# Kernel optimization log

Measured on AMD Instinct MI355X. Metric: run time of the kernel, lower is better.

The kernel has to match this reference:

```python
import jax, jax.numpy as jnp
import numpy as np

N = 50000
E = 800000
D = 128

def setup_inputs() -> dict:
    key = jax.random.key(0)
    ks = jax.random.split(key, 10)
    s = 1.0 / np.sqrt(D)
    return {
        "hidden": jax.random.normal(ks[0], (N, D), dtype=jnp.float32),
        "edge_index": jax.random.randint(ks[1], (2, E), 0, N, dtype=jnp.int64),
        "edge_attr": jax.random.uniform(ks[2], (E, 1), dtype=jnp.float32),
        # edge_encoder: Linear(1, D)
        "We": jax.random.uniform(ks[3], (1, D), minval=-1.0, maxval=1.0, dtype=jnp.float32),
        "be": jax.random.uniform(ks[4], (D,), minval=-1.0, maxval=1.0, dtype=jnp.float32),
        # mlp: Linear(D,D) -> ReLU -> Linear(D,D); weights stored [in,out]
        "W1": jax.random.uniform(ks[5], (D, D), minval=-s, maxval=s, dtype=jnp.float32),
        "b1": jax.random.uniform(ks[6], (D,), minval=-s, maxval=s, dtype=jnp.float32),
        "W2": jax.random.uniform(ks[7], (D, D), minval=-s, maxval=s, dtype=jnp.float32),
        "b2": jax.random.uniform(ks[8], (D,), minval=-s, maxval=s, dtype=jnp.float32),
        "eps": jnp.zeros((1,), dtype=jnp.float32),
    }

def reference(hidden, edge_index, edge_attr, We, be, W1, b1, W2, b2, eps):
    # NOTE: original forward computes relu(hidden) but discards it, passing
    # raw `hidden` into the conv; replicated faithfully.
    src, dst = edge_index[0], edge_index[1]
    edge_emb = edge_attr @ We + be                      # [E, D]
    msg = jax.nn.relu(hidden[src] + edge_emb)           # gather + message
    summed = jax.ops.segment_sum(msg, dst, num_segments=N)           # [N, D]
    cnt = jax.ops.segment_sum(jnp.ones((E,), hidden.dtype), dst, num_segments=N)
    aggr = summed / jnp.maximum(cnt, 1.0)[:, None]      # scatter-mean
    h = (1.0 + eps[0]) * hidden + aggr
    h = jax.nn.relu(h @ W1 + b1)
    out = h @ W2 + b2
    return out
```

## Files before the change

kernel.cpp:

```cpp
#include <hip/hip_runtime.h>

static constexpr int N_NODES = 50000;
static constexpr int D = 128;
static constexpr int E_EDGES = 800000;
static constexpr int SLOTS = 48;
static constexpr int TILES = N_NODES / 16;

static constexpr int NB   = 256;
static constexpr int BKW  = 196;
static constexpr int CAP  = 4096;
static constexpr int EPB  = 4096;
static constexpr int ABIN = (E_EDGES + EPB - 1) / EPB;
static constexpr int ACVT = (E_EDGES + 511) / 512;
static constexpr int AWPR = 8;

using half8   = __attribute__((ext_vector_type(8))) _Float16;
using half2v  = __attribute__((ext_vector_type(2))) _Float16;
using floatx4 = __attribute__((ext_vector_type(4))) float;

__global__ __launch_bounds__(512) void bin_coarse(
    const float* __restrict__ hidden,
    const int* __restrict__ edge_index,
    const float* __restrict__ edge_attr,
    const float* __restrict__ W1, const float* __restrict__ W2,
    _Float16* __restrict__ hidden16,
    _Float16* __restrict__ W1f, _Float16* __restrict__ W2f,
    int* __restrict__ bucketFill, int2* __restrict__ coarse)
{
    const int t = threadIdx.x;
    const int b = blockIdx.x;

    if (b >= ABIN + ACVT) {
        int p = (b - ABIN - ACVT) * 512 + t;
        int lane  = p & 63;
        int ntile = (p >> 6) & 7;
        int kstep = (p >> 9) & 3;
        int mat   = p >> 11;
        const float* W = mat ? W2 : W1;
        _Float16*   Wf = mat ? W2f : W1f;
        int n     = ntile * 16 + (lane & 15);
        int kbase = kstep * 32 + (lane >> 4) * 8;
        _Float16* dst = Wf + ((size_t)((kstep * 8 + ntile) * 64 + lane)) * 8;
        #pragma unroll
        for (int j = 0; j < 8; ++j)
            dst[j] = (_Float16)W[(size_t)(kbase + j) * D + n];
        return;
    }
    if (b >= ABIN) {
        int e = (b - ABIN) * 512 + t;
        if (e < N_NODES * D / 8) {
            float4 v0 = *((const float4*)hidden + 2 * (size_t)e);
            float4 v1 = *((const float4*)hidden + 2 * (size_t)e + 1);
            half8 o;
            o[0] = (_Float16)v0.x; o[1] = (_Float16)v0.y;
            o[2] = (_Float16)v0.z; o[3] = (_Float16)v0.w;
            o[4] = (_Float16)v1.x; o[5] = (_Float16)v1.y;
            o[6] = (_Float16)v1.z; o[7] = (_Float16)v1.w;
            ((half8*)hidden16)[e] = o;
        }
        return;
    }

    __shared__ int lcnt[NB];
    __shared__ int lbase[NB];
    if (t < NB) lcnt[t] = 0;
    __syncthreads();

    const int ebase = b * EPB;
    int src[8], bk[8], dl[8], rank[8];
    float at[8];
    #pragma unroll
    for (int k = 0; k < 8; ++k) {
        int e = ebase + k * 512 + t;
        bool v = e < E_EDGES;
        int d  = v ? edge_index[E_EDGES + e] : 0;
        src[k] = v ? edge_index[e] : 0;
        at[k]  = v ? edge_attr[e] : 0.f;
        bk[k]  = (int)((unsigned)d / (unsigned)BKW);
        dl[k]  = d - bk[k] * BKW;
        rank[k] = v ? 0 : -1;
    }
    #pragma unroll
    for (int k = 0; k < 8; ++k)
        if (rank[k] >= 0)
            rank[k] = atomicAdd(&lcnt[bk[k]], 1);
    __syncthreads();

    if (t < NB) {
        int c = lcnt[t];
        lbase[t] = (c > 0) ? atomicAdd(&bucketFill[t], c) : 0;
    }
    __syncthreads();

    #pragma unroll
    for (int k = 0; k < 8; ++k) {
        if (rank[k] >= 0) {
            int idx = lbase[bk[k]] + rank[k];
            if (idx < CAP)
                coarse[(size_t)bk[k] * CAP + idx] =
                    make_int2(src[k] | (dl[k] << 16), __float_as_int(at[k]));
        }
    }
}

__global__ __launch_bounds__(512) void bin_fine(
    const int2* __restrict__ coarse,
    const int* __restrict__ bucketFill,
    int* __restrict__ counts, int2* __restrict__ csr)
{
    __shared__ int2 tile[BKW * SLOTS];
    __shared__ int  lcnt[BKW];
    const int t  = threadIdx.x;
    const int b  = blockIdx.x;
    const int n0 = b * BKW;
    const int nn = min(N_NODES - n0, BKW);

    if (t < nn) lcnt[t] = 0;
    __syncthreads();

    const int cnt = min(__builtin_amdgcn_readfirstlane(bucketFill[b]), CAP);
    const int2* seg = coarse + (size_t)b * CAP;
    for (int r = t; r < cnt; r += 512) {
        int2 rec = seg[r];
        int d   = (rec.x >> 16) & 0xff;
        int pos = atomicAdd(&lcnt[d], 1);
        if (pos < SLOTS)
            tile[d * SLOTS + pos] = make_int2(rec.x & 0xffff, rec.y);
    }
    __syncthreads();

    int4* gout = (int4*)(csr + (size_t)n0 * SLOTS);
    const int4* tin = (const int4*)tile;
    const int nq = nn * SLOTS / 2;
    for (int i = t; i < nq; i += 512)
        gout[i] = tin[i];
    if (t < nn) counts[n0 + t] = lcnt[t];
}

__global__ __launch_bounds__(256) void fused_gather_mlp(
    const _Float16* __restrict__ hidden16,
    const int2* __restrict__ csr,
    const int* __restrict__ counts,
    const float* __restrict__ We, const float* __restrict__ be,
    const float* __restrict__ eps,
    const _Float16* __restrict__ W1f, const float* __restrict__ b1,
    const _Float16* __restrict__ W2f, const float* __restrict__ b2,
    float* __restrict__ out)
{
    __shared__ _Float16 hA[16 * 136];
    __shared__ _Float16 tB[16 * 136];
    const int tid  = threadIdx.x;
    const int wave = tid >> 6;
    const int lane = tid & 63;
    const int node0 = blockIdx.x * 16;
    const int d0 = lane << 1;

    const float2 wv = *(const float2*)(We + d0);
    const float2 bv = *(const float2*)(be + d0);
    const float onePlusEps = 1.0f + eps[0];

    const int nbase = node0 + __builtin_amdgcn_readfirstlane(wave << 2);
    const int4 c4 = *(const int4*)(counts + nbase);
    int dg[4];
    dg[0] = c4.x; dg[1] = c4.y; dg[2] = c4.z; dg[3] = c4.w;

    int m_[4], mc[4];
    const int2* ep[4];
    #pragma unroll
    for (int i = 0; i < 4; ++i) {
        m_[i] = min(dg[i], SLOTS);
        mc[i] = max(m_[i] - 1, 0);
        ep[i] = csr + (size_t)(nbase + i) * SLOTS;
    }
    float a0[4] = {0.f, 0.f, 0.f, 0.f};
    float a1[4] = {0.f, 0.f, 0.f, 0.f};
    const int mmax = max(max(m_[0], m_[1]), max(m_[2], m_[3]));

    #pragma unroll 2
    for (int j = 0; j < mmax; ++j) {
        #pragma unroll
        for (int i = 0; i < 4; ++i) {
            int2 rec = ep[i][min(j, mc[i])];
            int   src = min(max(rec.x, 0), N_NODES - 1);
            float at  = __int_as_float(rec.y);
            const float g = (j < m_[i]) ? 1.0f : 0.0f;
            half2v hp = *(const half2v*)(hidden16 + (size_t)src * D + d0);
            float t0 = fmaxf((float)hp.x + __builtin_fmaf(at, wv.x, bv.x), 0.f);
            float t1 = fmaxf((float)hp.y + __builtin_fmaf(at, wv.y, bv.y), 0.f);
            a0[i] = __builtin_fmaf(g, t0, a0[i]);
            a1[i] = __builtin_fmaf(g, t1, a1[i]);
        }
    }

    #pragma unroll
    for (int i = 0; i < 4; ++i) {
        const int row = (nbase - node0) + i;
        const float rin = 1.0f / fmaxf((float)dg[i], 1.0f);
        half2v hidp = *(const half2v*)(hidden16 + (size_t)(nbase + i) * D + d0);
        half2v o;
        o.x = (_Float16)(onePlusEps * (float)hidp.x + a0[i] * rin);
        o.y = (_Float16)(onePlusEps * (float)hidp.y + a1[i] * rin);
        *(half2v*)&hA[row * 136 + d0] = o;
    }
    __syncthreads();

    const int ln16 = lane & 15;
    const int quad = lane >> 4;

    half8 a[4];
    #pragma unroll
    for (int ks = 0; ks < 4; ++ks)
        a[ks] = *(const half8*)&hA[ln16 * 136 + ks * 32 + quad * 8];

    floatx4 acc[2];
    #pragma unroll
    for (int h = 0; h < 2; ++h) {
        const int nt = wave * 2 + h;
        float bb = b1[nt * 16 + ln16];
        acc[h] = (floatx4){bb, bb, bb, bb};
        #pragma unroll
        for (int ks = 0; ks < 4; ++ks) {
            half8 b = *(const half8*)(W1f + ((size_t)((ks * 8 + nt) * 64 + lane)) * 8);
            acc[h] = __builtin_amdgcn_mfma_f32_16x16x32_f16(a[ks], b, acc[h], 0, 0, 0);
        }
    }
    #pragma unroll
    for (int h = 0; h < 2; ++h) {
        const int nt = wave * 2 + h;
        #pragma unroll
        for (int r = 0; r < 4; ++r)
            tB[(quad * 4 + r) * 136 + nt * 16 + ln16] = (_Float16)fmaxf(acc[h][r], 0.f);
    }
    __syncthreads();

    #pragma unroll
    for (int ks = 0; ks < 4; ++ks)
        a[ks] = *(const half8*)&tB[ln16 * 136 + ks * 32 + quad * 8];

    #pragma unroll
    for (int h = 0; h < 2; ++h) {
        const int nt = wave * 2 + h;
        float bb = b2[nt * 16 + ln16];
        acc[h] = (floatx4){bb, bb, bb, bb};
        #pragma unroll
        for (int ks = 0; ks < 4; ++ks) {
            half8 b = *(const half8*)(W2f + ((size_t)((ks * 8 + nt) * 64 + lane)) * 8);
            acc[h] = __builtin_amdgcn_mfma_f32_16x16x32_f16(a[ks], b, acc[h], 0, 0, 0);
        }
    }
    #pragma unroll
    for (int h = 0; h < 2; ++h) {
        const int nt = wave * 2 + h;
        #pragma unroll
        for (int r = 0; r < 4; ++r)
            out[(size_t)(node0 + quad * 4 + r) * D + nt * 16 + ln16] = acc[h][r];
    }
}

extern "C" void kernel_launch(void* const* d_in, const int* in_sizes, int n_in,
                              void* d_out, int out_size, void* d_ws, size_t ws_size,
                              hipStream_t stream) {
    const float* hidden     = (const float*)d_in[0];
    const int*   edge_index = (const int*)d_in[1];
    const float* edge_attr  = (const float*)d_in[2];
    const float* We         = (const float*)d_in[3];
    const float* be         = (const float*)d_in[4];
    const float* W1         = (const float*)d_in[5];
    const float* b1         = (const float*)d_in[6];
    const float* W2         = (const float*)d_in[7];
    const float* b2         = (const float*)d_in[8];
    const float* eps        = (const float*)d_in[9];
    float* out = (float*)d_out;

    _Float16* hidden16   = (_Float16*)d_ws;
    _Float16* W1f        = hidden16 + (size_t)N_NODES * D;
    _Float16* W2f        = W1f + (size_t)D * D;
    int*      counts     = (int*)(W2f + (size_t)D * D);
    int2*     csr        = (int2*)(counts + N_NODES);
    int*      bucketFill = (int*)(csr + (size_t)N_NODES * SLOTS);
    int2*     coarse     = (int2*)(bucketFill + NB);

    hipMemsetAsync(bucketFill, 0, NB * sizeof(int), stream);

    bin_coarse<<<ABIN + ACVT + AWPR, 512, 0, stream>>>(
        hidden, edge_index, edge_attr, W1, W2, hidden16, W1f, W2f,
        bucketFill, coarse);

    bin_fine<<<NB, 512, 0, stream>>>(coarse, bucketFill, counts, csr);

    fused_gather_mlp<<<TILES, 256, 0, stream>>>(
        hidden16, csr, counts, We, be, eps, W1f, b1, W2f, b2, out);
}
```

Measured before the change: 152.2 us.

## Use 512-thread blocks with two nodes per wave and zero-padded CSR slots

The fused gather+MLP kernel now runs 8 waves per 16-node tile, so each wave gathers 2 nodes instead of 4 and computes one 16-column MFMA output tile instead of two. This shortens each wave's serial gather chain and exposes more memory parallelism per block. To remove per-edge clamping in the gather loop, bin_fine zero-fills the shared tile so unused CSR slots hold node 0 with weight 0. Those slots are then read unconditionally and masked by the gate factor. The cost is an extra shared-memory clear in bin_fine and wasted loads for padded slots.

```diff
diff --git a/kernel.cpp b/kernel.cpp
--- a/kernel.cpp
+++ b/kernel.cpp
@@ -115,6 +115,9 @@
     const int n0 = b * BKW;
     const int nn = min(N_NODES - n0, BKW);
 
+    int4* tz = (int4*)tile;
+    for (int i = t; i < BKW * SLOTS / 2; i += 512)
+        tz[i] = make_int4(0, 0, 0, 0);
     if (t < nn) lcnt[t] = 0;
     __syncthreads();
 
@@ -137,7 +140,7 @@
     if (t < nn) counts[n0 + t] = lcnt[t];
 }
 
-__global__ __launch_bounds__(256) void fused_gather_mlp(
+__global__ __launch_bounds__(512) void fused_gather_mlp(
     const _Float16* __restrict__ hidden16,
     const int2* __restrict__ csr,
     const int* __restrict__ counts,
@@ -159,29 +162,28 @@
     const float2 bv = *(const float2*)(be + d0);
     const float onePlusEps = 1.0f + eps[0];
 
-    const int nbase = node0 + __builtin_amdgcn_readfirstlane(wave << 2);
-    const int4 c4 = *(const int4*)(counts + nbase);
-    int dg[4];
-    dg[0] = c4.x; dg[1] = c4.y; dg[2] = c4.z; dg[3] = c4.w;
-
-    int m_[4], mc[4];
-    const int2* ep[4];
-    #pragma unroll
-    for (int i = 0; i < 4; ++i) {
+    const int nbase = node0 + __builtin_amdgcn_readfirstlane(wave << 1);
+    const int2 c2 = *(const int2*)(counts + nbase);
+    int dg[2];
+    dg[0] = c2.x; dg[1] = c2.y;
+
+    int m_[2];
+    const int2* ep[2];
+    #pragma unroll
+    for (int i = 0; i < 2; ++i) {
         m_[i] = min(dg[i], SLOTS);
-        mc[i] = max(m_[i] - 1, 0);
         ep[i] = csr + (size_t)(nbase + i) * SLOTS;
     }
-    float a0[4] = {0.f, 0.f, 0.f, 0.f};
-    float a1[4] = {0.f, 0.f, 0.f, 0.f};
-    const int mmax = max(max(m_[0], m_[1]), max(m_[2], m_[3]));
+    float a0[2] = {0.f, 0.f};
+    float a1[2] = {0.f, 0.f};
+    const int mmax = max(m_[0], m_[1]);
 
     #pragma unroll 2
     for (int j = 0; j < mmax; ++j) {
         #pragma unroll
-        for (int i = 0; i < 4; ++i) {
-            int2 rec = ep[i][min(j, mc[i])];
-            int   src = min(max(rec.x, 0), N_NODES - 1);
+        for (int i = 0; i < 2; ++i) {
+            int2 rec = ep[i][j];
+            int   src = rec.x;
             float at  = __int_as_float(rec.y);
             const float g = (j < m_[i]) ? 1.0f : 0.0f;
             half2v hp = *(const half2v*)(hidden16 + (size_t)src * D + d0);
@@ -193,7 +195,7 @@
     }
 
     #pragma unroll
-    for (int i = 0; i < 4; ++i) {
+    for (int i = 0; i < 2; ++i) {
         const int row = (nbase - node0) + i;
         const float rin = 1.0f / fmaxf((float)dg[i], 1.0f);
         half2v hidp = *(const half2v*)(hidden16 + (size_t)(nbase + i) * D + d0);
@@ -206,55 +208,44 @@
 
     const int ln16 = lane & 15;
     const int quad = lane >> 4;
+    const int nt   = wave;
 
     half8 a[4];
     #pragma unroll
     for (int ks = 0; ks < 4; ++ks)
         a[ks] = *(const half8*)&hA[ln16 * 136 + ks * 32 + quad * 8];
 
-    floatx4 acc[2];
-    #pragma unroll
-    for (int h = 0; h < 2; ++h) {
-        const int nt = wave * 2 + h;
+    floatx4 acc;
+    {
         float bb = b1[nt * 16 + ln16];
-        acc[h] = (floatx4){bb, bb, bb, bb};
+        acc = (floatx4){bb, bb, bb, bb};
         #pragma unroll
         for (int ks = 0; ks < 4; ++ks) {
             half8 b = *(const half8*)(W1f + ((size_t)((ks * 8 + nt) * 64 + lane)) * 8);
-            acc[h] = __builtin_amdgcn_mfma_f32_16x16x32_f16(a[ks], b, acc[h], 0, 0, 0);
-        }
-    }
-    #pragma unroll
-    for (int h = 0; h < 2; ++h) {
-        const int nt = wave * 2 + h;
-        #pragma unroll
-        for (int r = 0; r < 4; ++r)
-            tB[(quad * 4 + r) * 136 + nt * 16 + ln16] = (_Float16)fmaxf(acc[h][r], 0.f);
-    }
+            acc = __builtin_amdgcn_mfma_f32_16x16x32_f16(a[ks], b, acc, 0, 0, 0);
+        }
+    }
+    #pragma unroll
+    for (int r = 0; r < 4; ++r)
+        tB[(quad * 4 + r) * 136 + nt * 16 + ln16] = (_Float16)fmaxf(acc[r], 0.f);
     __syncthreads();
 
     #pragma unroll
     for (int ks = 0; ks < 4; ++ks)
         a[ks] = *(const half8*)&tB[ln16 * 136 + ks * 32 + quad * 8];
 
-    #pragma unroll
-    for (int h = 0; h < 2; ++h) {
-        const int nt = wave * 2 + h;
+    {
         float bb = b2[nt * 16 + ln16];
-        acc[h] = (floatx4){bb, bb, bb, bb};
+        acc = (floatx4){bb, bb, bb, bb};
         #pragma unroll
         for (int ks = 0; ks < 4; ++ks) {
             half8 b = *(const half8*)(W2f + ((size_t)((ks * 8 + nt) * 64 + lane)) * 8);
-            acc[h] = __builtin_amdgcn_mfma_f32_16x16x32_f16(a[ks], b, acc[h], 0, 0, 0);
-        }
-    }
-    #pragma unroll
-    for (int h = 0; h < 2; ++h) {
-        const int nt = wave * 2 + h;
-        #pragma unroll
-        for (int r = 0; r < 4; ++r)
-            out[(size_t)(node0 + quad * 4 + r) * D + nt * 16 + ln16] = acc[h][r];
-    }
+            acc = __builtin_amdgcn_mfma_f32_16x16x32_f16(a[ks], b, acc, 0, 0, 0);
+        }
+    }
+    #pragma unroll
+    for (int r = 0; r < 4; ++r)
+        out[(size_t)(node0 + quad * 4 + r) * D + nt * 16 + ln16] = acc[r];
 }
 
 extern "C" void kernel_launch(void* const* d_in, const int* in_sizes, int n_in,
@@ -288,6 +279,6 @@
 
     bin_fine<<<NB, 512, 0, stream>>>(coarse, bucketFill, counts, csr);
 
-    fused_gather_mlp<<<TILES, 256, 0, stream>>>(
+    fused_gather_mlp<<<TILES, 512, 0, stream>>>(
         hidden16, csr, counts, We, be, eps, W1f, b1, W2f, b2, out);
 }
```

Result: no change. 152.9 us (+0.5%).
